# Performance work log

Hardware: AMD Instinct MI355X
Metric: run time of the kernel (lower is better)

The kernel has to match this reference:

```python
import jax, jax.numpy as jnp
from jax import lax
import numpy as np

S = 2048      # seq_len
E = 1024      # embedding_dim
H = 512       # hidden per direction (hidden_dim // 2)
V = 50000     # vocab
T = 16        # tagset_size
START, STOP = 0, 1
NEG = -10000.0


def setup_inputs() -> dict:
    key = jax.random.key(0)
    ks = jax.random.split(key, 20)
    bound = 1.0 / np.sqrt(H)

    def u(k, shape):
        return jax.random.uniform(k, shape, minval=-bound, maxval=bound, dtype=jnp.float32)

    sentence = jax.random.randint(ks[0], (S,), 0, V)
    emb = jax.random.normal(ks[1], (V, E), dtype=jnp.float32) * 0.1
    # PyTorch LSTM weights, gate order (i, f, g, o) stacked along first dim
    Wih_f = u(ks[2], (4 * H, E)); Whh_f = u(ks[3], (4 * H, H))
    bih_f = u(ks[4], (4 * H,));   bhh_f = u(ks[5], (4 * H,))
    Wih_b = u(ks[6], (4 * H, E)); Whh_b = u(ks[7], (4 * H, H))
    bih_b = u(ks[8], (4 * H,));   bhh_b = u(ks[9], (4 * H,))
    # init_hidden(): randn initial (h0, c0), [2 directions, H] (batch=1 squeezed)
    h0 = jax.random.normal(ks[10], (2, H), dtype=jnp.float32)
    c0 = jax.random.normal(ks[11], (2, H), dtype=jnp.float32)
    Wout = u(ks[12], (T, 2 * H)); bout = u(ks[13], (T,))
    transitions = jax.random.normal(ks[14], (T, T), dtype=jnp.float32)
    transitions = transitions.at[START, :].set(NEG).at[:, STOP].set(NEG)
    return dict(sentence=sentence, emb=emb,
                Wih_f=Wih_f, Whh_f=Whh_f, bih_f=bih_f, bhh_f=bhh_f,
                Wih_b=Wih_b, Whh_b=Whh_b, bih_b=bih_b, bhh_b=bhh_b,
                h0=h0, c0=c0, Wout=Wout, bout=bout, transitions=transitions)


def _lstm_dir(x, Wih, Whh, bih, bhh, h0, c0):
    # x: [S, E] -> hs: [S, H]; PyTorch gate order i, f, g, o
    xg = x @ Wih.T + bih + bhh  # precompute input contribution [S, 4H]

    def step(carry, xg_t):
        h, c = carry
        g = xg_t + h @ Whh.T
        i, f, gg, o = jnp.split(g, 4)
        i, f, o = jax.nn.sigmoid(i), jax.nn.sigmoid(f), jax.nn.sigmoid(o)
        c = f * c + i * jnp.tanh(gg)
        h = o * jnp.tanh(c)
        return (h, c), h

    _, hs = lax.scan(step, (h0, c0), xg)
    return hs


def _feats(sentence, emb, Wih_f, Whh_f, bih_f, bhh_f, Wih_b, Whh_b, bih_b, bhh_b,
           h0, c0, Wout, bout):
    x = emb[sentence]  # [S, E]
    hf = _lstm_dir(x, Wih_f, Whh_f, bih_f, bhh_f, h0[0], c0[0])              # [S, H]
    hb = _lstm_dir(x[::-1], Wih_b, Whh_b, bih_b, bhh_b, h0[1], c0[1])[::-1]  # [S, H]
    out = jnp.concatenate([hf, hb], axis=-1)  # [S, 2H]
    return out @ Wout.T + bout                # [S, T]


def _viterbi(feats, transitions):
    v0 = jnp.full((T,), NEG, dtype=feats.dtype).at[START].set(0.0)

    def vstep(v, feat):
        scores = v[None, :] + transitions        # [T(next), T(prev)]
        bp = jnp.argmax(scores, axis=1)          # best prev tag per next tag
        v_new = jnp.max(scores, axis=1) + feat
        return v_new, bp

    v, bps = lax.scan(vstep, v0, feats)          # bps: [S, T]
    terminal = v + transitions[STOP]
    best = jnp.argmax(terminal)
    path_score = terminal[best]

    def btstep(tag, bp):
        return bp[tag], tag

    _, path = lax.scan(btstep, best, bps, reverse=True)  # path[t] = tag at t
    return path_score, path


def reference(sentence, emb, Wih_f, Whh_f, bih_f, bhh_f, Wih_b, Whh_b, bih_b, bhh_b,
              h0, c0, Wout, bout, transitions):
    feats = _feats(sentence, emb, Wih_f, Whh_f, bih_f, bhh_f,
                   Wih_b, Whh_b, bih_b, bhh_b, h0, c0, Wout, bout)
    path_score, path = _viterbi(feats, transitions)
    return path_score, path
```

## Files before the change

### kernel.cpp

```cpp
#include <hip/hip_runtime.h>
#include <hip/hip_bf16.h>

#define S 2048
#define NEGV -10000.0f

typedef unsigned long long ull;
typedef unsigned int uint4v __attribute__((ext_vector_type(4)));

__device__ __forceinline__ float fsig(float x) {
  return 1.0f / (1.0f + __expf(-x));
}
__device__ __forceinline__ float ftanh(float x) {
  float a = fabsf(x);
  float e = __expf(-2.0f * a);
  float r = (1.0f - e) / (1.0f + e);
  return copysignf(r, x);
}

__global__ void init_k(const float* __restrict__ h0, ull* __restrict__ hbuf,
                       int* __restrict__ flags) {
  int b = blockIdx.x, u = threadIdx.x;
  if (b < 2) {
    ull pk = (1ULL << 32) | (ull)__float_as_uint(h0[b * 512 + u]);
    __hip_atomic_store(&hbuf[b * 1024 + u], pk, __ATOMIC_RELAXED, __HIP_MEMORY_SCOPE_AGENT);
    __hip_atomic_store(&hbuf[b * 1024 + 512 + u], 0ULL, __ATOMIC_RELAXED, __HIP_MEMORY_SCOPE_AGENT);
  } else {
    flags[(b - 2) * 512 + u] = 0;
  }
}

__global__ __launch_bounds__(256) void fused_k(
    const int* __restrict__ sent, const float* __restrict__ emb,
    const float* __restrict__ Wih_f, const float* __restrict__ Wih_b,
    const float* __restrict__ bih_f, const float* __restrict__ bhh_f,
    const float* __restrict__ bih_b, const float* __restrict__ bhh_b,
    const float* __restrict__ Whh_f, const float* __restrict__ Whh_b,
    const float* __restrict__ c0,
    float* __restrict__ xg,
    ull* __restrict__ hbuf,
    float* __restrict__ hs_cat,
    int* __restrict__ flags)
{
  __shared__ __align__(16) float smem[4544];
  const int t = threadIdx.x;

  if (blockIdx.x >= 128) {
    float* Asm = smem;
    float* Bsm = smem + 2304;
    int*   sidx = (int*)(smem + 4480);
    const int tm = t >> 4, tn = t & 15;
    const int lr = t >> 2, lkq = t & 3;

    for (int i = 0; i < 16; ++i) {
      const int T = (blockIdx.x - 128) + 128 * i;
      const int byo = T >> 6, bxo = T & 63;
      const int by = (byo & 1) ? (31 - (byo >> 1)) : (byo >> 1);
      const int bx = (bxo & 1) ? (32 + (bxo >> 1)) : (bxo >> 1);
      const int n0 = bx * 64, m0 = by * 64;

      const float* W = (n0 < 2048) ? (Wih_f + (size_t)n0 * 1024)
                                   : (Wih_b + (size_t)(n0 - 2048) * 1024);
      __syncthreads();
      if (t < 64) sidx[t] = sent[m0 + t];
      __syncthreads();

      float acc[4][4] = {};
      for (int k0 = 0; k0 < 1024; k0 += 32) {
        const float* ap = emb + (size_t)sidx[lr] * 1024 + k0 + lkq * 8;
        float4 a0 = *(const float4*)ap;
        float4 a1 = *(const float4*)(ap + 4);
        const float* bp = W + (size_t)lr * 1024 + k0 + lkq * 8;
        float4 b0 = *(const float4*)bp;
        float4 b1 = *(const float4*)(bp + 4);
        __syncthreads();
        *(float4*)&Asm[lr * 36 + lkq * 8]     = a0;
        *(float4*)&Asm[lr * 36 + lkq * 8 + 4] = a1;
        {
          const float* bb0 = (const float*)&b0;
          const float* bb1 = (const float*)&b1;
          #pragma unroll
          for (int j = 0; j < 4; ++j) Bsm[(lkq * 8 + j) * 68 + lr] = bb0[j];
          #pragma unroll
          for (int j = 0; j < 4; ++j) Bsm[(lkq * 8 + 4 + j) * 68 + lr] = bb1[j];
        }
        __syncthreads();
        #pragma unroll
        for (int kk = 0; kk < 32; ++kk) {
          float a0_ = Asm[(tm * 4 + 0) * 36 + kk];
          float a1_ = Asm[(tm * 4 + 1) * 36 + kk];
          float a2_ = Asm[(tm * 4 + 2) * 36 + kk];
          float a3_ = Asm[(tm * 4 + 3) * 36 + kk];
          float4 bv = *(const float4*)&Bsm[kk * 68 + tn * 4];
          acc[0][0] = fmaf(a0_, bv.x, acc[0][0]); acc[0][1] = fmaf(a0_, bv.y, acc[0][1]);
          acc[0][2] = fmaf(a0_, bv.z, acc[0][2]); acc[0][3] = fmaf(a0_, bv.w, acc[0][3]);
          acc[1][0] = fmaf(a1_, bv.x, acc[1][0]); acc[1][1] = fmaf(a1_, bv.y, acc[1][1]);
          acc[1][2] = fmaf(a1_, bv.z, acc[1][2]); acc[1][3] = fmaf(a1_, bv.w, acc[1][3]);
          acc[2][0] = fmaf(a2_, bv.x, acc[2][0]); acc[2][1] = fmaf(a2_, bv.y, acc[2][1]);
          acc[2][2] = fmaf(a2_, bv.z, acc[2][2]); acc[2][3] = fmaf(a2_, bv.w, acc[2][3]);
          acc[3][0] = fmaf(a3_, bv.x, acc[3][0]); acc[3][1] = fmaf(a3_, bv.y, acc[3][1]);
          acc[3][2] = fmaf(a3_, bv.z, acc[3][2]); acc[3][3] = fmaf(a3_, bv.w, acc[3][3]);
        }
      }

      const float* bi = (n0 < 2048) ? bih_f : bih_b;
      const float* bh = (n0 < 2048) ? bhh_f : bhh_b;
      const int nb = (n0 < 2048) ? n0 : (n0 - 2048);
      #pragma unroll
      for (int ii = 0; ii < 4; ++ii) {
        int m = m0 + tm * 4 + ii;
        #pragma unroll
        for (int j = 0; j < 4; ++j) {
          int nn = tn * 4 + j;
          float bias = bi[nb + nn] + bh[nb + nn];
          __hip_atomic_store(&xg[(size_t)m * 4096 + n0 + nn], acc[ii][j] + bias,
                             __ATOMIC_RELAXED, __HIP_MEMORY_SCOPE_AGENT);
        }
      }
      asm volatile("s_waitcnt vmcnt(0)" ::: "memory");
      __syncthreads();
      if (t == 0)
        __hip_atomic_store(&flags[by * 64 + bx], 1, __ATOMIC_RELAXED, __HIP_MEMORY_SCOPE_AGENT);
    }
    return;
  }

  const int w = blockIdx.x;
  const int dir = w & 1;
  const int wid = w >> 1;
  const int rr = t >> 3;
  const int seg = t & 7;
  const int g  = rr & 3;
  const int ul = rr >> 2;
  const int unit = wid * 8 + ul;
  const int grow = g * 512 + unit;
  const int bxf  = dir * 32 + g * 8 + (wid >> 3);

  float (*h_lds)[544] = (float(*)[544])smem;

  const float* Whh = dir ? Whh_b : Whh_f;
  float wreg[64];
  {
    const float* src = Whh + (size_t)grow * 512 + seg * 64;
    #pragma unroll
    for (int j = 0; j < 16; ++j) {
      float4 v = *(const float4*)(src + j * 4);
      wreg[4 * j + 0] = v.x; wreg[4 * j + 1] = v.y;
      wreg[4 * j + 2] = v.z; wreg[4 * j + 3] = v.w;
    }
  }

  ull* hb = hbuf + dir * 1024;
  float c_reg = c0[dir * 512 + unit];

  const int u0 = t * 2;
  const int wchunk = u0 >> 6, wpos = u0 & 63;

  float xg_a = 0.0f, xg_b = 0.0f;
  if (seg == 0) {
    int by0 = dir ? 31 : 0;
    while (__hip_atomic_load(&flags[by0 * 64 + bxf], __ATOMIC_RELAXED,
                             __HIP_MEMORY_SCOPE_AGENT) != 1)
      __builtin_amdgcn_s_sleep(8);
    int r0 = dir ? (S - 1) : 0;
    int r1 = dir ? (S - 2) : 1;
    xg_a = __hip_atomic_load(&xg[(size_t)r0 * 4096 + dir * 2048 + grow],
                             __ATOMIC_RELAXED, __HIP_MEMORY_SCOPE_AGENT);
    xg_b = __hip_atomic_load(&xg[(size_t)r1 * 4096 + dir * 2048 + grow],
                             __ATOMIC_RELAXED, __HIP_MEMORY_SCOPE_AGENT);
  }

  #define LSTM_STEP(K, XG_REG)                                                  \
  {                                                                             \
    const int k = (K);                                                          \
    float xgv = XG_REG;                                                         \
    if (seg == 0 && k + 2 < S) {            \
      int rowk = dir ? (S - 3 - k) : (k + 2);                                   \
      if ((rowk & 63) == (dir ? 63 : 0)) {       \
        int byn = rowk >> 6;                                                    \
        while (__hip_atomic_load(&flags[byn * 64 + bxf], __ATOMIC_RELAXED,      \
                                 __HIP_MEMORY_SCOPE_AGENT) != 1)                \
          __builtin_amdgcn_s_sleep(8);                                          \
      }                                                                         \
      XG_REG = __hip_atomic_load(&xg[(size_t)rowk * 4096 + dir * 2048 + grow],  \
                                 __ATOMIC_RELAXED, __HIP_MEMORY_SCOPE_AGENT);   \
    }                                                                           \
         \
    {                                                                           \
      ull* src = hb + (k & 1) * 512 + u0;                                       \
      const unsigned want = (unsigned)(k + 1);                                  \
      uint4v v;                                                                 \
      asm volatile("global_load_dwordx4 %0, %1, off sc0 sc1"                    \
                   : "=v"(v) : "v"(src) : "memory");                            \
      asm volatile("s_waitcnt vmcnt(0)" ::: "memory");                          \
      while (v.y != want || v.w != want) {                                      \
        __builtin_amdgcn_s_sleep(1);                                            \
        asm volatile("global_load_dwordx4 %0, %1, off sc0 sc1"                  \
                     : "=v"(v) : "v"(src) : "memory");                          \
        asm volatile("s_waitcnt vmcnt(0)" ::: "memory");                        \
      }                                                                         \
      float* dst = &h_lds[k & 1][wchunk * 68 + wpos];                           \
      dst[0] = __uint_as_float(v.x);                                            \
      dst[1] = __uint_as_float(v.z);                                            \
    }                                                                           \
    __syncthreads();                                                            \
                                         \
    const float* hl = &h_lds[k & 1][0];                                         \
    float p0 = 0.f, p1 = 0.f, p2 = 0.f, p3 = 0.f;                               \
    const float4* h4 = (const float4*)(hl + seg * 68);                          \
    _Pragma("unroll")                                                           \
    for (int j = 0; j < 16; ++j) {                                              \
      float4 hv = h4[j];                                                        \
      p0 = fmaf(wreg[4 * j + 0], hv.x, p0);                                     \
      p1 = fmaf(wreg[4 * j + 1], hv.y, p1);                                     \
      p2 = fmaf(wreg[4 * j + 2], hv.z, p2);                                     \
      p3 = fmaf(wreg[4 * j + 3], hv.w, p3);                                     \
    }                                                                           \
    float p = (p0 + p1) + (p2 + p3) + xgv;                                      \
    p += __shfl_xor(p, 1);                                                      \
    p += __shfl_xor(p, 2);                                                      \
    p += __shfl_xor(p, 4);                                                      \
    float gb_ = __shfl_xor(p, 8);                                 \
    float gc_ = __shfl_xor(p, 16);                                \
    float gd_ = __shfl_xor(gb_, 16);                              \
    if (g == 0) {                                                               \
      float iv = fsig(p), fv = fsig(gb_), ov = fsig(gd_);                       \
      float gv = ftanh(gc_);                                                    \
      c_reg = fv * c_reg + iv * gv;                                             \
      float hv = ov * ftanh(c_reg);                                             \
      if (seg == 0) {                                                           \
        ull pk = ((ull)(unsigned)(k + 2) << 32) | (ull)__float_as_uint(hv);     \
        __hip_atomic_store(&hb[((k + 1) & 1) * 512 + unit], pk,                 \
                           __ATOMIC_RELAXED, __HIP_MEMORY_SCOPE_AGENT);         \
        int orig = dir ? (S - 1 - k) : k;                                       \
        hs_cat[(size_t)orig * 1024 + dir * 512 + unit] = hv;                    \
      }                                                                         \
    }                                                                           \
  }

  for (int kk = 0; kk < S; kk += 2) {
    LSTM_STEP(kk, xg_a);
    LSTM_STEP(kk + 1, xg_b);
  }
  #undef LSTM_STEP
}

__global__ __launch_bounds__(64) void feats_k(
    const float* __restrict__ hs_cat, const float* __restrict__ Wout,
    const float* __restrict__ bout, float* __restrict__ feats)
{
  int tpos = blockIdx.x;
  int l = threadIdx.x;
  int j = l & 15, q = l >> 4;
  const float* h = hs_cat + (size_t)tpos * 1024 + q * 256;
  const float* wv = Wout + (size_t)j * 1024 + q * 256;
  float s = 0.f;
  #pragma unroll 8
  for (int i = 0; i < 256; i += 4) {
    float4 hv = *(const float4*)(h + i);
    float4 ww = *(const float4*)(wv + i);
    s = fmaf(hv.x, ww.x, s); s = fmaf(hv.y, ww.y, s);
    s = fmaf(hv.z, ww.z, s); s = fmaf(hv.w, ww.w, s);
  }
  s += __shfl_xor(s, 16);
  s += __shfl_xor(s, 32);
  if (q == 0) feats[tpos * 16 + j] = s + bout[j];
}

__device__ __forceinline__ ull compose_map(ull a, ull b) {
  ull r = 0;
  #pragma unroll
  for (int i = 0; i < 16; ++i) {
    int bi = (int)((b >> (4 * i)) & 15);
    int ai = (int)((a >> (4 * bi)) & 15);
    r |= (ull)ai << (4 * i);
  }
  return r;
}

__device__ __forceinline__ ull spread16(ull x) {
  x &= 0xFFFFULL;
  x = (x | (x << 24)) & 0x000000FF000000FFULL;
  x = (x | (x << 12)) & 0x000F000F000F000FULL;
  x = (x | (x << 6))  & 0x0303030303030303ULL;
  x = (x | (x << 3))  & 0x1111111111111111ULL;
  return x;
}

__global__ __launch_bounds__(64, 1) void viterbi_k(
    const float* __restrict__ feats, const float* __restrict__ trans,
    float* __restrict__ out)
{
  __shared__ ull bpm[S];
  const int l = threadIdx.x;
  const int next = l & 15, q4 = (l >> 4) * 4;

  const float tr0 = trans[next * 16 + q4 + 0];
  const float tr1 = trans[next * 16 + q4 + 1];
  const float tr2 = trans[next * 16 + q4 + 2];
  const float tr3 = trans[next * 16 + q4 + 3];

  float vcur = (next == 0) ? 0.0f : NEGV;

  #define VSTEP(T, FREG)                                                        \
  {                                                                             \
    float pv0 = __shfl(vcur, q4 + 0, 16);                                       \
    float pv1 = __shfl(vcur, q4 + 1, 16);                                       \
    float pv2 = __shfl(vcur, q4 + 2, 16);                                       \
    float pv3 = __shfl(vcur, q4 + 3, 16);                                       \
    float m = pv0 + tr0; int mi = q4;                                           \
    float s1 = pv1 + tr1; if (s1 > m) { m = s1; mi = q4 + 1; }                  \
    float s2 = pv2 + tr2; if (s2 > m) { m = s2; mi = q4 + 2; }                  \
    float s3 = pv3 + tr3; if (s3 > m) { m = s3; mi = q4 + 3; }                  \
    { float om = __shfl_xor(m, 16); int omi = __shfl_xor(mi, 16);               \
      if (om > m || (om == m && omi < mi)) { m = om; mi = omi; } }              \
    { float om = __shfl_xor(m, 32); int omi = __shfl_xor(mi, 32);               \
      if (om > m || (om == m && omi < mi)) { m = om; mi = omi; } }              \
    vcur = m + (FREG);                                                          \
    ull b0 = __ballot(mi & 1) & 0xFFFFULL;                                      \
    ull b1 = __ballot(mi & 2) & 0xFFFFULL;                                      \
    ull b2 = __ballot(mi & 4) & 0xFFFFULL;                                      \
    ull b3 = __ballot(mi & 8) & 0xFFFFULL;                                      \
    ull map = spread16(b0) | (spread16(b1) << 1) |                              \
              (spread16(b2) << 2) | (spread16(b3) << 3);                        \
    if (l == 0) bpm[T] = map;                                                   \
  }

  float f0 = feats[0 * 16 + next], f1 = feats[1 * 16 + next];
  float f2 = feats[2 * 16 + next], f3 = feats[3 * 16 + next];
  float f4 = feats[4 * 16 + next], f5 = feats[5 * 16 + next];
  float f6 = feats[6 * 16 + next], f7 = feats[7 * 16 + next];

  for (int t = 0; t < S; t += 8) {
    VSTEP(t + 0, f0); if (t + 8  < S) f0 = feats[(t + 8)  * 16 + next];
    VSTEP(t + 1, f1); if (t + 9  < S) f1 = feats[(t + 9)  * 16 + next];
    VSTEP(t + 2, f2); if (t + 10 < S) f2 = feats[(t + 10) * 16 + next];
    VSTEP(t + 3, f3); if (t + 11 < S) f3 = feats[(t + 11) * 16 + next];
    VSTEP(t + 4, f4); if (t + 12 < S) f4 = feats[(t + 12) * 16 + next];
    VSTEP(t + 5, f5); if (t + 13 < S) f5 = feats[(t + 13) * 16 + next];
    VSTEP(t + 6, f6); if (t + 14 < S) f6 = feats[(t + 14) * 16 + next];
    VSTEP(t + 7, f7); if (t + 15 < S) f7 = feats[(t + 15) * 16 + next];
  }
  #undef VSTEP

  float term = vcur + trans[16 + next];
  int ti = next;
  #pragma unroll
  for (int mask = 1; mask <= 8; mask <<= 1) {
    float om = __shfl_xor(term, mask);
    int omi = __shfl_xor(ti, mask);
    if (om > term || (om == term && omi < ti)) { term = om; ti = omi; }
  }

  __syncthreads();

  ull M = bpm[32 * l + 31];
  for (int i = 30; i >= 0; --i) M = compose_map(bpm[32 * l + i], M);

  ull Sm = M;
  #pragma unroll
  for (int d = 1; d < 64; d <<= 1) {
    ull o = __shfl_down(Sm, d);
    if (l + d < 64) Sm = compose_map(Sm, o);
  }
  ull G = __shfl_down(Sm, 1);
  if (l == 63) G = 0xFEDCBA9876543210ULL;

  int cur = (int)((G >> (4 * ti)) & 15);
  for (int i = 31; i >= 1; --i) {
    int t = 32 * l + i;
    out[1 + t] = (float)cur;
    cur = (int)((bpm[t] >> (4 * cur)) & 15);
  }
  out[1 + 32 * l] = (float)cur;
  if (l == 0) out[0] = term;
}

extern "C" void kernel_launch(void* const* d_in, const int* in_sizes, int n_in,
                              void* d_out, int out_size, void* d_ws, size_t ws_size,
                              hipStream_t stream) {
  const int*   sent  = (const int*)d_in[0];
  const float* emb   = (const float*)d_in[1];
  const float* Wih_f = (const float*)d_in[2];
  const float* Whh_f = (const float*)d_in[3];
  const float* bih_f = (const float*)d_in[4];
  const float* bhh_f = (const float*)d_in[5];
  const float* Wih_b = (const float*)d_in[6];
  const float* Whh_b = (const float*)d_in[7];
  const float* bih_b = (const float*)d_in[8];
  const float* bhh_b = (const float*)d_in[9];
  const float* h0    = (const float*)d_in[10];
  const float* c0    = (const float*)d_in[11];
  const float* Wout  = (const float*)d_in[12];
  const float* bout  = (const float*)d_in[13];
  const float* trans = (const float*)d_in[14];
  float* out = (float*)d_out;

  char* ws = (char*)d_ws;
  float* xg     = (float*)(ws);
  float* hs_cat = (float*)(ws + 33554432);
  float* feats  = (float*)(ws + 41943040);
  ull*   hbuf   = (ull*)  (ws + 42074112);
  int*   flags  = (int*)  (ws + 42090496);

  init_k<<<6, 512, 0, stream>>>(h0, hbuf, flags);
  fused_k<<<256, 256, 0, stream>>>(sent, emb, Wih_f, Wih_b, bih_f, bhh_f,
                                   bih_b, bhh_b, Whh_f, Whh_b, c0,
                                   xg, hbuf, hs_cat, flags);
  feats_k<<<2048, 64, 0, stream>>>(hs_cat, Wout, bout, feats);
  viterbi_k<<<1, 64, 0, stream>>>(feats, trans, out);
}
```

Measured before the change: 3.919 ms.

## Fuse output projection into persistent LSTM kernel and pipeline hidden-state polling

The separate feats kernel is removed. After the recurrence, LSTM blocks bump a global completion counter, every block spins until all 128 recurrent blocks finish, and then all 256 blocks compute the Wout projection for 8 positions each. The hidden-state spin loop also changes to keep two outstanding loads in flight, alternating between them, so a fresh value can arrive sooner after the producer writes it. Savings are one kernel launch plus some polling latency on the critical recurrence chain. The cost is a grid-wide spin barrier, which depends on all 256 blocks being co-resident, and extra memory traffic from the polling.

```diff
diff --git a/kernel.cpp b/kernel.cpp
--- a/kernel.cpp
+++ b/kernel.cpp
@@ -25,7 +25,9 @@
     __hip_atomic_store(&hbuf[b * 1024 + u], pk, __ATOMIC_RELAXED, __HIP_MEMORY_SCOPE_AGENT);
     __hip_atomic_store(&hbuf[b * 1024 + 512 + u], 0ULL, __ATOMIC_RELAXED, __HIP_MEMORY_SCOPE_AGENT);
   } else {
-    flags[(b - 2) * 512 + u] = 0;
+    __hip_atomic_store(&flags[(b - 2) * 512 + u], 0, __ATOMIC_RELAXED, __HIP_MEMORY_SCOPE_AGENT);
+    if (b == 2 && u == 0)
+      __hip_atomic_store(&flags[2048], 0, __ATOMIC_RELAXED, __HIP_MEMORY_SCOPE_AGENT);
   }
 }
 
@@ -36,9 +38,11 @@
     const float* __restrict__ bih_b, const float* __restrict__ bhh_b,
     const float* __restrict__ Whh_f, const float* __restrict__ Whh_b,
     const float* __restrict__ c0,
+    const float* __restrict__ Wout, const float* __restrict__ bout,
     float* __restrict__ xg,
     ull* __restrict__ hbuf,
     float* __restrict__ hs_cat,
+    float* __restrict__ feats,
     int* __restrict__ flags)
 {
   __shared__ __align__(16) float smem[4544];
@@ -121,149 +125,176 @@
       if (t == 0)
         __hip_atomic_store(&flags[by * 64 + bx], 1, __ATOMIC_RELAXED, __HIP_MEMORY_SCOPE_AGENT);
     }
-    return;
-  }
-
-  const int w = blockIdx.x;
-  const int dir = w & 1;
-  const int wid = w >> 1;
-  const int rr = t >> 3;
-  const int seg = t & 7;
-  const int g  = rr & 3;
-  const int ul = rr >> 2;
-  const int unit = wid * 8 + ul;
-  const int grow = g * 512 + unit;
-  const int bxf  = dir * 32 + g * 8 + (wid >> 3);
-
-  float (*h_lds)[544] = (float(*)[544])smem;
-
-  const float* Whh = dir ? Whh_b : Whh_f;
-  float wreg[64];
+  } else {
+    const int w = blockIdx.x;
+    const int dir = w & 1;
+    const int wid = w >> 1;
+    const int rr = t >> 3;
+    const int seg = t & 7;
+    const int g  = rr & 3;
+    const int ul = rr >> 2;
+    const int unit = wid * 8 + ul;
+    const int grow = g * 512 + unit;
+    const int bxf  = dir * 32 + g * 8 + (wid >> 3);
+
+    float (*h_lds)[544] = (float(*)[544])smem;
+
+    const float* Whh = dir ? Whh_b : Whh_f;
+    float wreg[64];
+    {
+      const float* src = Whh + (size_t)grow * 512 + seg * 64;
+      #pragma unroll
+      for (int j = 0; j < 16; ++j) {
+        float4 v = *(const float4*)(src + j * 4);
+        wreg[4 * j + 0] = v.x; wreg[4 * j + 1] = v.y;
+        wreg[4 * j + 2] = v.z; wreg[4 * j + 3] = v.w;
+      }
+    }
+
+    ull* hb = hbuf + dir * 1024;
+    float c_reg = c0[dir * 512 + unit];
+
+    const int u0 = t * 2;
+    const int wchunk = u0 >> 6, wpos = u0 & 63;
+
+    float xg_a = 0.0f, xg_b = 0.0f;
+    if (seg == 0) {
+      int by0 = dir ? 31 : 0;
+      while (__hip_atomic_load(&flags[by0 * 64 + bxf], __ATOMIC_RELAXED,
+                               __HIP_MEMORY_SCOPE_AGENT) != 1)
+        __builtin_amdgcn_s_sleep(8);
+      int r0 = dir ? (S - 1) : 0;
+      int r1 = dir ? (S - 2) : 1;
+      xg_a = __hip_atomic_load(&xg[(size_t)r0 * 4096 + dir * 2048 + grow],
+                               __ATOMIC_RELAXED, __HIP_MEMORY_SCOPE_AGENT);
+      xg_b = __hip_atomic_load(&xg[(size_t)r1 * 4096 + dir * 2048 + grow],
+                               __ATOMIC_RELAXED, __HIP_MEMORY_SCOPE_AGENT);
+    }
+
+    #define LSTM_STEP(K, XG_REG)                                                  \
+    {                                                                             \
+      const int k = (K);                                                          \
+      float xgv = XG_REG;                                                         \
+      if (seg == 0 && k + 2 < S) {            \
+        int rowk = dir ? (S - 3 - k) : (k + 2);                                   \
+        if ((rowk & 63) == (dir ? 63 : 0)) {       \
+          int byn = rowk >> 6;                                                    \
+          while (__hip_atomic_load(&flags[byn * 64 + bxf], __ATOMIC_RELAXED,      \
+                                   __HIP_MEMORY_SCOPE_AGENT) != 1)                \
+            __builtin_amdgcn_s_sleep(8);                                          \
+        }                                                                         \
+        XG_REG = __hip_atomic_load(&xg[(size_t)rowk * 4096 + dir * 2048 + grow],  \
+                                   __ATOMIC_RELAXED, __HIP_MEMORY_SCOPE_AGENT);   \
+      }                                                                           \
+          \
+      {                                                                           \
+        ull* src = hb + (k & 1) * 512 + u0;                                       \
+        const unsigned want = (unsigned)(k + 1);                                  \
+        uint4v va, vb;                                                            \
+        asm volatile("s_waitcnt vmcnt(0)" ::: "memory");    \
+        asm volatile("global_load_dwordx4 %0, %1, off sc0 sc1"                    \
+                     : "=v"(va) : "v"(src) : "memory");                           \
+        __builtin_amdgcn_s_sleep(4);                            \
+        asm volatile("global_load_dwordx4 %0, %1, off sc0 sc1"                    \
+                     : "=v"(vb) : "v"(src) : "memory");                           \
+        for (;;) {                                                                \
+          asm volatile("s_waitcnt vmcnt(1)" : "+v"(va) :: "memory");              \
+          if (va.y == want && va.w == want) {                                     \
+            asm volatile("s_waitcnt vmcnt(0)" : "+v"(va) :: "memory");            \
+            vb = va; break;                                                       \
+          }                                                                       \
+          __builtin_amdgcn_s_sleep(2);                                            \
+          asm volatile("global_load_dwordx4 %0, %1, off sc0 sc1"                  \
+                       : "=v"(va) : "v"(src) : "memory");                         \
+          asm volatile("s_waitcnt vmcnt(1)" : "+v"(vb) :: "memory");              \
+          if (vb.y == want && vb.w == want) {                                     \
+            asm volatile("s_waitcnt vmcnt(0)" : "+v"(vb) :: "memory");            \
+            break;                                                                \
+          }                                                                       \
+          __builtin_amdgcn_s_sleep(2);                                            \
+          asm volatile("global_load_dwordx4 %0, %1, off sc0 sc1"                  \
+                       : "=v"(vb) : "v"(src) : "memory");                         \
+        }                                                                         \
+        float* dst = &h_lds[k & 1][wchunk * 68 + wpos];                           \
+        dst[0] = __uint_as_float(vb.x);                                           \
+        dst[1] = __uint_as_float(vb.z);                                           \
+      }                                                                           \
+      __syncthreads();                                                            \
+                                           \
+      const float* hl = &h_lds[k & 1][0];                                         \
+      float p0 = 0.f, p1 = 0.f, p2 = 0.f, p3 = 0.f;                               \
+      const float4* h4 = (const float4*)(hl + seg * 68);                          \
+      _Pragma("unroll")                                                           \
+      for (int j = 0; j < 16; ++j) {                                              \
+        float4 hv = h4[j];                                                        \
+        p0 = fmaf(wreg[4 * j + 0], hv.x, p0);                                     \
+        p1 = fmaf(wreg[4 * j + 1], hv.y, p1);                                     \
+        p2 = fmaf(wreg[4 * j + 2], hv.z, p2);                                     \
+        p3 = fmaf(wreg[4 * j + 3], hv.w, p3);                                     \
+      }                                                                           \
+      float p = (p0 + p1) + (p2 + p3) + xgv;                                      \
+      p += __shfl_xor(p, 1);                                                      \
+      p += __shfl_xor(p, 2);                                                      \
+      p += __shfl_xor(p, 4);                                                      \
+      float gb_ = __shfl_xor(p, 8);                                 \
+      float gc_ = __shfl_xor(p, 16);                                \
+      float gd_ = __shfl_xor(gb_, 16);                              \
+      if (g == 0) {                                                               \
+        float iv = fsig(p), fv = fsig(gb_), ov = fsig(gd_);                       \
+        float gv = ftanh(gc_);                                                    \
+        c_reg = fv * c_reg + iv * gv;                                             \
+        float hv = ov * ftanh(c_reg);                                             \
+        if (seg == 0) {                                                           \
+          ull pk = ((ull)(unsigned)(k + 2) << 32) | (ull)__float_as_uint(hv);     \
+          __hip_atomic_store(&hb[((k + 1) & 1) * 512 + unit], pk,                 \
+                             __ATOMIC_RELAXED, __HIP_MEMORY_SCOPE_AGENT);         \
+          int orig = dir ? (S - 1 - k) : k;                                       \
+          __hip_atomic_store(&hs_cat[(size_t)orig * 1024 + dir * 512 + unit], hv, \
+                             __ATOMIC_RELAXED, __HIP_MEMORY_SCOPE_AGENT);         \
+        }                                                                         \
+      }                                                                           \
+    }
+
+    for (int kk = 0; kk < S; kk += 2) {
+      LSTM_STEP(kk, xg_a);
+      LSTM_STEP(kk + 1, xg_b);
+    }
+    #undef LSTM_STEP
+
+    asm volatile("s_waitcnt vmcnt(0)" ::: "memory");
+    __syncthreads();
+    if (t == 0)
+      __hip_atomic_fetch_add(&flags[2048], 1, __ATOMIC_RELAXED, __HIP_MEMORY_SCOPE_AGENT);
+  }
+
+  if (t == 0) {
+    while (__hip_atomic_load(&flags[2048], __ATOMIC_RELAXED,
+                             __HIP_MEMORY_SCOPE_AGENT) != 128)
+      __builtin_amdgcn_s_sleep(32);
+  }
+  __syncthreads();
   {
-    const float* src = Whh + (size_t)grow * 512 + seg * 64;
+    const int l = t & 63;
+    const int wv4 = t >> 6;
+    const int j = l & 15, q = l >> 4;
     #pragma unroll
-    for (int j = 0; j < 16; ++j) {
-      float4 v = *(const float4*)(src + j * 4);
-      wreg[4 * j + 0] = v.x; wreg[4 * j + 1] = v.y;
-      wreg[4 * j + 2] = v.z; wreg[4 * j + 3] = v.w;
-    }
-  }
-
-  ull* hb = hbuf + dir * 1024;
-  float c_reg = c0[dir * 512 + unit];
-
-  const int u0 = t * 2;
-  const int wchunk = u0 >> 6, wpos = u0 & 63;
-
-  float xg_a = 0.0f, xg_b = 0.0f;
-  if (seg == 0) {
-    int by0 = dir ? 31 : 0;
-    while (__hip_atomic_load(&flags[by0 * 64 + bxf], __ATOMIC_RELAXED,
-                             __HIP_MEMORY_SCOPE_AGENT) != 1)
-      __builtin_amdgcn_s_sleep(8);
-    int r0 = dir ? (S - 1) : 0;
-    int r1 = dir ? (S - 2) : 1;
-    xg_a = __hip_atomic_load(&xg[(size_t)r0 * 4096 + dir * 2048 + grow],
-                             __ATOMIC_RELAXED, __HIP_MEMORY_SCOPE_AGENT);
-    xg_b = __hip_atomic_load(&xg[(size_t)r1 * 4096 + dir * 2048 + grow],
-                             __ATOMIC_RELAXED, __HIP_MEMORY_SCOPE_AGENT);
-  }
-
-  #define LSTM_STEP(K, XG_REG)                                                  \
-  {                                                                             \
-    const int k = (K);                                                          \
-    float xgv = XG_REG;                                                         \
-    if (seg == 0 && k + 2 < S) {            \
-      int rowk = dir ? (S - 3 - k) : (k + 2);                                   \
-      if ((rowk & 63) == (dir ? 63 : 0)) {       \
-        int byn = rowk >> 6;                                                    \
-        while (__hip_atomic_load(&flags[byn * 64 + bxf], __ATOMIC_RELAXED,      \
-                                 __HIP_MEMORY_SCOPE_AGENT) != 1)                \
-          __builtin_amdgcn_s_sleep(8);                                          \
-      }                                                                         \
-      XG_REG = __hip_atomic_load(&xg[(size_t)rowk * 4096 + dir * 2048 + grow],  \
-                                 __ATOMIC_RELAXED, __HIP_MEMORY_SCOPE_AGENT);   \
-    }                                                                           \
-         \
-    {                                                                           \
-      ull* src = hb + (k & 1) * 512 + u0;                                       \
-      const unsigned want = (unsigned)(k + 1);                                  \
-      uint4v v;                                                                 \
-      asm volatile("global_load_dwordx4 %0, %1, off sc0 sc1"                    \
-                   : "=v"(v) : "v"(src) : "memory");                            \
-      asm volatile("s_waitcnt vmcnt(0)" ::: "memory");                          \
-      while (v.y != want || v.w != want) {                                      \
-        __builtin_amdgcn_s_sleep(1);                                            \
-        asm volatile("global_load_dwordx4 %0, %1, off sc0 sc1"                  \
-                     : "=v"(v) : "v"(src) : "memory");                          \
-        asm volatile("s_waitcnt vmcnt(0)" ::: "memory");                        \
-      }                                                                         \
-      float* dst = &h_lds[k & 1][wchunk * 68 + wpos];                           \
-      dst[0] = __uint_as_float(v.x);                                            \
-      dst[1] = __uint_as_float(v.z);                                            \
-    }                                                                           \
-    __syncthreads();                                                            \
-                                         \
-    const float* hl = &h_lds[k & 1][0];                                         \
-    float p0 = 0.f, p1 = 0.f, p2 = 0.f, p3 = 0.f;                               \
-    const float4* h4 = (const float4*)(hl + seg * 68);                          \
-    _Pragma("unroll")                                                           \
-    for (int j = 0; j < 16; ++j) {                                              \
-      float4 hv = h4[j];                                                        \
-      p0 = fmaf(wreg[4 * j + 0], hv.x, p0);                                     \
-      p1 = fmaf(wreg[4 * j + 1], hv.y, p1);                                     \
-      p2 = fmaf(wreg[4 * j + 2], hv.z, p2);                                     \
-      p3 = fmaf(wreg[4 * j + 3], hv.w, p3);                                     \
-    }                                                                           \
-    float p = (p0 + p1) + (p2 + p3) + xgv;                                      \
-    p += __shfl_xor(p, 1);                                                      \
-    p += __shfl_xor(p, 2);                                                      \
-    p += __shfl_xor(p, 4);                                                      \
-    float gb_ = __shfl_xor(p, 8);                                 \
-    float gc_ = __shfl_xor(p, 16);                                \
-    float gd_ = __shfl_xor(gb_, 16);                              \
-    if (g == 0) {                                                               \
-      float iv = fsig(p), fv = fsig(gb_), ov = fsig(gd_);                       \
-      float gv = ftanh(gc_);                                                    \
-      c_reg = fv * c_reg + iv * gv;                                             \
-      float hv = ov * ftanh(c_reg);                                             \
-      if (seg == 0) {                                                           \
-        ull pk = ((ull)(unsigned)(k + 2) << 32) | (ull)__float_as_uint(hv);     \
-        __hip_atomic_store(&hb[((k + 1) & 1) * 512 + unit], pk,                 \
-                           __ATOMIC_RELAXED, __HIP_MEMORY_SCOPE_AGENT);         \
-        int orig = dir ? (S - 1 - k) : k;                                       \
-        hs_cat[(size_t)orig * 1024 + dir * 512 + unit] = hv;                    \
-      }                                                                         \
-    }                                                                           \
-  }
-
-  for (int kk = 0; kk < S; kk += 2) {
-    LSTM_STEP(kk, xg_a);
-    LSTM_STEP(kk + 1, xg_b);
-  }
-  #undef LSTM_STEP
-}
-
-__global__ __launch_bounds__(64) void feats_k(
-    const float* __restrict__ hs_cat, const float* __restrict__ Wout,
-    const float* __restrict__ bout, float* __restrict__ feats)
-{
-  int tpos = blockIdx.x;
-  int l = threadIdx.x;
-  int j = l & 15, q = l >> 4;
-  const float* h = hs_cat + (size_t)tpos * 1024 + q * 256;
-  const float* wv = Wout + (size_t)j * 1024 + q * 256;
-  float s = 0.f;
-  #pragma unroll 8
-  for (int i = 0; i < 256; i += 4) {
-    float4 hv = *(const float4*)(h + i);
-    float4 ww = *(const float4*)(wv + i);
-    s = fmaf(hv.x, ww.x, s); s = fmaf(hv.y, ww.y, s);
-    s = fmaf(hv.z, ww.z, s); s = fmaf(hv.w, ww.w, s);
-  }
-  s += __shfl_xor(s, 16);
-  s += __shfl_xor(s, 32);
-  if (q == 0) feats[tpos * 16 + j] = s + bout[j];
+    for (int r = 0; r < 2; ++r) {
+      const int tpos = blockIdx.x * 8 + wv4 * 2 + r;
+      const float* h = hs_cat + (size_t)tpos * 1024 + q * 256;
+      const float* wp = Wout + (size_t)j * 1024 + q * 256;
+      float s = 0.f;
+      #pragma unroll 8
+      for (int i = 0; i < 256; i += 4) {
+        float4 hv = *(const float4*)(h + i);
+        float4 ww = *(const float4*)(wp + i);
+        s = fmaf(hv.x, ww.x, s); s = fmaf(hv.y, ww.y, s);
+        s = fmaf(hv.z, ww.z, s); s = fmaf(hv.w, ww.w, s);
+      }
+      s += __shfl_xor(s, 16);
+      s += __shfl_xor(s, 32);
+      if (q == 0) feats[tpos * 16 + j] = s + bout[j];
+    }
+  }
 }
 
 __device__ __forceinline__ ull compose_map(ull a, ull b) {
@@ -404,8 +435,7 @@
 
   init_k<<<6, 512, 0, stream>>>(h0, hbuf, flags);
   fused_k<<<256, 256, 0, stream>>>(sent, emb, Wih_f, Wih_b, bih_f, bhh_f,
-                                   bih_b, bhh_b, Whh_f, Whh_b, c0,
-                                   xg, hbuf, hs_cat, flags);
-  feats_k<<<2048, 64, 0, stream>>>(hs_cat, Wout, bout, feats);
+                                   bih_b, bhh_b, Whh_f, Whh_b, c0, Wout, bout,
+                                   xg, hbuf, hs_cat, feats, flags);
   viterbi_k<<<1, 64, 0, stream>>>(feats, trans, out);
 }
```

Result: slower. 4.726 ms (+20.6%).
